# Kernel optimization log

Measured on AMD Instinct MI355X. Metric: run time of the kernel, lower is better.

The kernel has to match this reference:

```python
import jax, jax.numpy as jnp
import numpy as np

H, O, E, V = 128, 128, 512, 34
B, T, L = 64, 2048, 256


def _lstm(x, wih, whh, bih, bhh):
    # x: [T, B, Din] -> outputs [T, B, H]; PyTorch gate order i, f, g, o
    n = whh.shape[1]
    h0 = jnp.zeros((x.shape[1], n), x.dtype)
    b = bih + bhh
    def step(carry, xt):
        h, c = carry
        g = xt @ wih.T + h @ whh.T + b
        i, f, gg, o = jnp.split(g, 4, axis=-1)
        c = jax.nn.sigmoid(f) * c + jax.nn.sigmoid(i) * jnp.tanh(gg)
        h = jax.nn.sigmoid(o) * jnp.tanh(c)
        return (h, c), h
    _, ys = jax.lax.scan(step, (h0, h0), x)
    return ys


def _conv1d_s2(x, w, b):
    # x: [B, Cin, T], w: [Cout, Cin, 2], kernel=2 stride=2 valid
    y = jax.lax.conv_general_dilated(x, w, (2,), 'VALID', dimension_numbers=('NCH', 'OIH', 'NCH'))
    return y + b[None, :, None]


def setup_inputs():
    key = jax.random.key(0)
    ctr = [0]
    def mk(shape, s=0.05):
        ctr[0] += 1
        return jax.random.normal(jax.random.fold_in(key, ctr[0]), shape, dtype=jnp.float32) * s
    inp = {}
    inp['utter'] = mk((B, T, 40), 1.0)
    inp['targets'] = jax.random.randint(jax.random.fold_in(key, 999), (B, L), 0, V)
    inp['wih_f'] = mk((4 * H, 40)); inp['whh_f'] = mk((4 * H, H)); inp['bih_f'] = mk((4 * H,)); inp['bhh_f'] = mk((4 * H,))
    inp['wih_r'] = mk((4 * H, 40)); inp['whh_r'] = mk((4 * H, H)); inp['bih_r'] = mk((4 * H,)); inp['bhh_r'] = mk((4 * H,))
    inp['c1w'] = mk((H, 2 * H, 2)); inp['c1b'] = mk((H,))
    inp['wih1'] = mk((4 * H, H)); inp['whh1'] = mk((4 * H, H)); inp['bih1'] = mk((4 * H,)); inp['bhh1'] = mk((4 * H,))
    inp['c2w'] = mk((H, H, 2)); inp['c2b'] = mk((H,))
    inp['wih2'] = mk((4 * H, H)); inp['whh2'] = mk((4 * H, H)); inp['bih2'] = mk((4 * H,)); inp['bhh2'] = mk((4 * H,))
    inp['kw'] = mk((O, H)); inp['kb'] = mk((O,)); inp['vw'] = mk((O, H)); inp['vb'] = mk((O,))
    inp['wihd'] = mk((4 * O, O + E)); inp['whhd'] = mk((4 * O, O)); inp['bihd'] = mk((4 * O,)); inp['bhhd'] = mk((4 * O,))
    inp['w1'] = mk((V, O)); inp['b1'] = mk((V,)); inp['w2'] = mk((V, O)); inp['b2'] = mk((V,))
    inp['w3'] = mk((V, V)); inp['b3'] = mk((V,))
    inp['emb'] = mk((V, E), 1.0)
    inp['sh0'] = mk((B, O)); inp['sc0'] = mk((B, O))
    return inp


def _forward(utter, targets, wih_f, whh_f, bih_f, bhh_f, wih_r, whh_r, bih_r, bhh_r,
             c1w, c1b, wih1, whh1, bih1, bhh1, c2w, c2b, wih2, whh2, bih2, bhh2,
             kw, kb, vw, vb, wihd, whhd, bihd, bhhd, w1, b1, w2, b2, w3, b3,
             emb, sh0, sc0):
    # ---- Listener (encoder) ----
    x = jnp.transpose(utter, (1, 0, 2))            # [T, B, 40]
    fwd = _lstm(x, wih_f, whh_f, bih_f, bhh_f)
    bwd = _lstm(x[::-1], wih_r, whh_r, bih_r, bhh_r)[::-1]
    h = jnp.concatenate([fwd, bwd], axis=-1)       # [T, B, 2H]
    h = jnp.transpose(h, (1, 2, 0))                # [B, 2H, T]
    h = _conv1d_s2(h, c1w, c1b)                    # [B, H, T/2]
    h = jnp.transpose(h, (2, 0, 1))                # [T/2, B, H]
    h = _lstm(h, wih1, whh1, bih1, bhh1)
    h = jnp.transpose(h, (1, 2, 0))
    h = _conv1d_s2(h, c2w, c2b)                    # [B, H, T/4]
    h = jnp.transpose(h, (2, 0, 1))
    h = _lstm(h, wih2, whh2, bih2, bhh2)
    h = jnp.transpose(h, (1, 0, 2))                # [B, T/4, H]
    hk = h @ kw.T + kb                              # [B, T/4, O]
    hv = h @ vw.T + vb
    # ---- Speller (decoder) ----
    ys = jnp.transpose(emb[targets], (1, 0, 2))[:-1]   # [L-1, B, E]
    mask = jnp.ones((utter.shape[0], hk.shape[1]), utter.dtype)  # all full-length
    bd = bihd + bhhd
    def step(carry, y_in):
        c, sh, sc = carry
        g = jnp.concatenate([y_in, c], axis=1) @ wihd.T + sh @ whhd.T + bd
        i, f, gg, o = jnp.split(g, 4, axis=-1)
        sc_n = jax.nn.sigmoid(f) * sc + jax.nn.sigmoid(i) * jnp.tanh(gg)
        sh_n = jax.nn.sigmoid(o) * jnp.tanh(sc_n)
        # NOTE: original attends with the cell state sc (faithful to source)
        att = jax.nn.softmax(jnp.einsum('btd,bd->bt', hk, sc_n), axis=1) * mask
        att = att / jnp.sum(att, axis=1, keepdims=True)
        c_n = jnp.einsum('bt,btd->bd', att, hv)
        out = jax.nn.relu(sh_n @ w1.T + b1 + c_n @ w2.T + b2)
        out = jax.nn.softmax(out @ w3.T + b3, axis=1)
        return (c_n, sh_n, sc_n), out
    c0 = jnp.zeros_like(sh0)
    _, preds = jax.lax.scan(step, (c0, sh0, sc0), ys)
    return jnp.transpose(preds, (1, 0, 2))         # [B, L-1, V]


def reference(utter, targets, wih_f, whh_f, bih_f, bhh_f, wih_r, whh_r, bih_r, bhh_r,
              c1w, c1b, wih1, whh1, bih1, bhh1, c2w, c2b, wih2, whh2, bih2, bhh2,
              kw, kb, vw, vb, wihd, whhd, bihd, bhhd, w1, b1, w2, b2, w3, b3,
              emb, sh0, sc0):
    return _forward(utter, targets, wih_f, whh_f, bih_f, bhh_f, wih_r, whh_r, bih_r, bhh_r,
                    c1w, c1b, wih1, whh1, bih1, bhh1, c2w, c2b, wih2, whh2, bih2, bhh2,
                    kw, kb, vw, vb, wihd, whhd, bihd, bhhd, w1, b1, w2, b2, w3, b3,
                    emb, sh0, sc0)
```

## Files before the change

### kernel.cpp

```cpp
#include <hip/hip_runtime.h>

typedef _Float16 half_t;
typedef _Float16 __attribute__((ext_vector_type(2))) half2_t;

__device__ __forceinline__ float fdot2_(half2_t a, half2_t b, float c) {
#if __has_builtin(__builtin_amdgcn_fdot2)
    return __builtin_amdgcn_fdot2(a, b, c, false);
#else
    return c + (float)a[0] * (float)b[0] + (float)a[1] * (float)b[1];
#endif
}
__device__ __forceinline__ half2_t h2(float a, float b) {
    half2_t r; r[0] = (half_t)a; r[1] = (half_t)b; return r;
}
__device__ __forceinline__ half2_t bc2(unsigned int u) {
    return __builtin_bit_cast(half2_t, u);
}
__device__ __forceinline__ unsigned int pk2(float a, float b) {
    return __builtin_bit_cast(unsigned int, h2(a, b));
}
__device__ __forceinline__ float sigm(float x) { return 1.0f / (1.0f + __expf(-x)); }
__device__ __forceinline__ float tanh_(float x) { return 1.0f - 2.0f / (1.0f + __expf(2.0f * x)); }
__device__ __forceinline__ unsigned int packbf2(float a, float b) {
    unsigned int ua = __float_as_uint(a);
    ua = (ua + 0x7fffu + ((ua >> 16) & 1u)) >> 16;
    unsigned int ub = __float_as_uint(b);
    ub = (ub + 0x7fffu + ((ub >> 16) & 1u)) >> 16;
    return ua | (ub << 16);
}
__device__ __forceinline__ float blo(unsigned int u) { return __uint_as_float(u << 16); }
__device__ __forceinline__ float bhi(unsigned int u) { return __uint_as_float(u & 0xffff0000u); }

__global__ __launch_bounds__(512, 1) void lstm1_k(
    const float* __restrict__ utter,
    const float* __restrict__ wih_f, const float* __restrict__ whh_f,
    const float* __restrict__ bih_f, const float* __restrict__ bhh_f,
    const float* __restrict__ wih_r, const float* __restrict__ whh_r,
    const float* __restrict__ bih_r, const float* __restrict__ bhh_r,
    unsigned short* __restrict__ Hf, unsigned short* __restrict__ Hr)
{
    const int tid = threadIdx.x;
    const int b   = blockIdx.x & 63;
    const int dir = blockIdx.x >> 6;
    const float* wih = dir ? wih_r : wih_f;
    const float* whh = dir ? whh_r : whh_f;
    const float* bih = dir ? bih_r : bih_f;
    const float* bhh = dir ? bhh_r : bhh_f;
    unsigned short* Hout = dir ? Hr : Hf;

    __shared__ float acts[512];
    __shared__ __align__(16) half_t h_h[128];
    __shared__ __align__(16) half_t x2[3][48];

    const int j = tid;
    const int gt = tid >> 7;
    unsigned int wr2[64];
    {
        const float4* wp = reinterpret_cast<const float4*>(whh + j * 128);
#pragma unroll
        for (int m = 0; m < 32; ++m) {
            float4 v = wp[m];
            wr2[2 * m]     = pk2(v.x, v.y);
            wr2[2 * m + 1] = pk2(v.z, v.w);
        }
    }
    unsigned int wx2[20];
    {
        const float4* xp = reinterpret_cast<const float4*>(wih + j * 40);
#pragma unroll
        for (int q = 0; q < 10; ++q) {
            float4 v = xp[q];
            wx2[2 * q]     = pk2(v.x, v.y);
            wx2[2 * q + 1] = pk2(v.z, v.w);
        }
    }
    const float bias = bih[j] + bhh[j];
    float c = 0.0f;
    if (tid < 128) h_h[tid] = (half_t)0.0f;
    if (tid < 40) {
        int tt0 = dir ? 2047 : 0;
        x2[0][tid] = (half_t)utter[((size_t)b * 2048 + tt0) * 40 + tid];
    } else if (tid < 80) {
        int tt1 = dir ? 2046 : 1;
        x2[1][tid - 40] = (half_t)utter[((size_t)b * 2048 + tt1) * 40 + (tid - 40)];
    }
    __syncthreads();

    for (int t = 0; t < 2048; ++t) {
        const int cur = t % 3;
        const int nx2 = (t + 2) % 3;
        float xn = 0.0f;
        const int tq = tid - 128;
        if (tq >= 0 && tq < 40) {
            int tn = (t + 2 < 2048) ? (t + 2) : 2047;
            int ttn = dir ? (2047 - tn) : tn;
            xn = utter[((size_t)b * 2048 + ttn) * 40 + tq];
        }
        float g0 = bias, g1 = 0.f, g2 = 0.f, g3 = 0.f;
        {
            const uint4* x4p = reinterpret_cast<const uint4*>(&x2[cur][0]);
#pragma unroll
            for (int q = 0; q < 5; ++q) {
                uint4 u = x4p[q];
                g0 = fdot2_(bc2(wx2[4 * q]),     bc2(u.x), g0);
                g1 = fdot2_(bc2(wx2[4 * q + 1]), bc2(u.y), g1);
                g2 = fdot2_(bc2(wx2[4 * q + 2]), bc2(u.z), g2);
                g3 = fdot2_(bc2(wx2[4 * q + 3]), bc2(u.w), g3);
            }
            const uint4* h4p = reinterpret_cast<const uint4*>(h_h);
#pragma unroll
            for (int q = 0; q < 16; ++q) {
                uint4 u = h4p[q];
                g0 = fdot2_(bc2(wr2[4 * q]),     bc2(u.x), g0);
                g1 = fdot2_(bc2(wr2[4 * q + 1]), bc2(u.y), g1);
                g2 = fdot2_(bc2(wr2[4 * q + 2]), bc2(u.z), g2);
                g3 = fdot2_(bc2(wr2[4 * q + 3]), bc2(u.w), g3);
            }
        }
        float g = (g0 + g1) + (g2 + g3);
        acts[j] = (gt == 2) ? tanh_(g) : sigm(g);
        __syncthreads();
        if (tid < 128) {
            float i_ = acts[tid];
            float f_ = acts[128 + tid];
            float g_ = acts[256 + tid];
            float o_ = acts[384 + tid];
            c = f_ * c + i_ * g_;
            float hh = o_ * tanh_(c);
            half_t hx = (half_t)hh;
            h_h[tid] = hx;
            int tt = dir ? (2047 - t) : t;
            Hout[((size_t)tt * 64 + b) * 128 + tid] = __builtin_bit_cast(unsigned short, hx);
        } else if (tq < 40) {
            x2[nx2][tq] = (half_t)xn;
        }
        __syncthreads();
    }
}

__global__ __launch_bounds__(512, 1) void lstm_k(
    const unsigned short* __restrict__ Ph,
    const float* __restrict__ whh,
    void* __restrict__ Hout, int T, int outHalf)
{
    const int tid = threadIdx.x;
    const int b = blockIdx.x;
    const int j = tid;
    const int gt = tid >> 7;
    __shared__ float acts[512];
    __shared__ __align__(16) half_t h_h[128];
    unsigned int wr2[64];
    {
        const float4* wp = reinterpret_cast<const float4*>(whh + j * 128);
#pragma unroll
        for (int m = 0; m < 32; ++m) {
            float4 v = wp[m];
            wr2[2 * m]     = pk2(v.x, v.y);
            wr2[2 * m + 1] = pk2(v.z, v.w);
        }
    }
    float c = 0.0f;
    if (tid < 128) h_h[tid] = (half_t)0.0f;
    const size_t pbase = (size_t)b * T;
    float p_cur = (float)__builtin_bit_cast(half_t, Ph[(pbase + 0) * 512 + j]);
    float p_n1  = (float)__builtin_bit_cast(half_t, Ph[(pbase + 1) * 512 + j]);
    __syncthreads();
    for (int t = 0; t < T; ++t) {
        int tn = (t + 2 < T) ? (t + 2) : (T - 1);
        float p_n2 = (float)__builtin_bit_cast(half_t, Ph[(pbase + tn) * 512 + j]);
        float g0 = p_cur, g1 = 0.f, g2 = 0.f, g3 = 0.f;
        const uint4* h4p = reinterpret_cast<const uint4*>(h_h);
#pragma unroll
        for (int q = 0; q < 16; ++q) {
            uint4 u = h4p[q];
            g0 = fdot2_(bc2(wr2[4 * q]),     bc2(u.x), g0);
            g1 = fdot2_(bc2(wr2[4 * q + 1]), bc2(u.y), g1);
            g2 = fdot2_(bc2(wr2[4 * q + 2]), bc2(u.z), g2);
            g3 = fdot2_(bc2(wr2[4 * q + 3]), bc2(u.w), g3);
        }
        float g = (g0 + g1) + (g2 + g3);
        acts[j] = (gt == 2) ? tanh_(g) : sigm(g);
        __syncthreads();
        if (tid < 128) {
            float i_ = acts[tid];
            float f_ = acts[128 + tid];
            float g_ = acts[256 + tid];
            float o_ = acts[384 + tid];
            c = f_ * c + i_ * g_;
            float hh = o_ * tanh_(c);
            half_t hx = (half_t)hh;
            h_h[tid] = hx;
            size_t oi = ((size_t)t * 64 + b) * 128 + tid;
            if (outHalf) ((unsigned short*)Hout)[oi] = __builtin_bit_cast(unsigned short, hx);
            else         ((float*)Hout)[oi] = hh;
        }
        __syncthreads();
        p_cur = p_n1;
        p_n1 = p_n2;
    }
}

template <int CIN>
__global__ __launch_bounds__(128) void conv_k(
    const unsigned short* __restrict__ HA, const unsigned short* __restrict__ HB,
    const float* __restrict__ W, const float* __restrict__ bias,
    float* __restrict__ out, int Tout)
{
    __shared__ __align__(16) float xin[64 * CIN];
    const int b = blockIdx.x;
    const int t0 = blockIdx.y * 32;
    const int tid = threadIdx.x;
    for (int idx = tid; idx < 64 * CIN; idx += 128) {
        int tl = idx / CIN, ci = idx % CIN;
        int tau = t0 * 2 + tl;
        unsigned short u;
        if constexpr (CIN == 256) {
            u = (ci < 128) ? HA[(size_t)tau * 8192 + b * 128 + ci]
                           : HB[(size_t)tau * 8192 + b * 128 + (ci - 128)];
        } else {
            u = HA[(size_t)tau * 8192 + b * 128 + ci];
        }
        xin[idx] = (float)__builtin_bit_cast(half_t, u);
    }
    __syncthreads();
    const int co = tid;
    float acc[32];
#pragma unroll
    for (int u = 0; u < 32; ++u) acc[u] = 0.0f;
    const float4* Wrow4 = reinterpret_cast<const float4*>(W + (size_t)co * 2 * CIN);
    const float4* xin4 = reinterpret_cast<const float4*>(xin);
    for (int c4 = 0; c4 < CIN / 4; ++c4) {
        float4 wA = Wrow4[2 * c4];
        float4 wB = Wrow4[2 * c4 + 1];
#pragma unroll
        for (int u = 0; u < 32; ++u) {
            float4 x0 = xin4[(2 * u) * (CIN / 4) + c4];
            float4 x1 = xin4[(2 * u + 1) * (CIN / 4) + c4];
            acc[u] += wA.x * x0.x + wA.y * x1.x + wA.z * x0.y + wA.w * x1.y
                    + wB.x * x0.z + wB.y * x1.z + wB.z * x0.w + wB.w * x1.w;
        }
    }
    float bs = bias[co];
#pragma unroll
    for (int u = 0; u < 32; ++u)
        out[((size_t)b * Tout + t0 + u) * 128 + co] = acc[u] + bs;
}

__global__ __launch_bounds__(256) void gemm_k(
    const float* __restrict__ A, const float* __restrict__ W, int ldw,
    const float* __restrict__ bias1, const float* __restrict__ bias2,
    void* __restrict__ C, int M, int N, int K, int mode, int Tdim)
{
    __shared__ __align__(16) float As[16][68];
    __shared__ __align__(16) float Ws[16][68];
    const int tid = threadIdx.x;
    const int m0 = blockIdx.x * 64, n0 = blockIdx.y * 64;
    const int kk = tid & 15, mm = tid >> 4;
    const int tm = tid & 15, tn = tid >> 4;
    float acc[4][4];
#pragma unroll
    for (int i = 0; i < 4; ++i)
#pragma unroll
        for (int jj = 0; jj < 4; ++jj) acc[i][jj] = 0.0f;

    for (int k0 = 0; k0 < K; k0 += 16) {
#pragma unroll
        for (int r = 0; r < 4; ++r) {
            As[kk][mm + 16 * r] = A[(size_t)(m0 + mm + 16 * r) * K + k0 + kk];
            Ws[kk][mm + 16 * r] = W[(size_t)(n0 + mm + 16 * r) * ldw + k0 + kk];
        }
        __syncthreads();
#pragma unroll
        for (int q = 0; q < 16; ++q) {
            float4 a = reinterpret_cast<const float4*>(&As[q][0])[tm];
            float4 w = reinterpret_cast<const float4*>(&Ws[q][0])[tn];
            acc[0][0] += a.x * w.x; acc[0][1] += a.x * w.y; acc[0][2] += a.x * w.z; acc[0][3] += a.x * w.w;
            acc[1][0] += a.y * w.x; acc[1][1] += a.y * w.y; acc[1][2] += a.y * w.z; acc[1][3] += a.y * w.w;
            acc[2][0] += a.z * w.x; acc[2][1] += a.z * w.y; acc[2][2] += a.z * w.z; acc[2][3] += a.z * w.w;
            acc[3][0] += a.w * w.x; acc[3][1] += a.w * w.y; acc[3][2] += a.w * w.z; acc[3][3] += a.w * w.w;
        }
        __syncthreads();
    }
    float bv[4];
#pragma unroll
    for (int jj = 0; jj < 4; ++jj) {
        int n = n0 + tn * 4 + jj;
        float v = 0.0f;
        if (bias1) v += bias1[n];
        if (bias2) v += bias2[n];
        bv[jj] = v;
    }
#pragma unroll
    for (int i = 0; i < 4; ++i) {
        int m = m0 + tm * 4 + i;
#pragma unroll
        for (int jj = 0; jj < 4; ++jj) {
            int n = n0 + tn * 4 + jj;
            float v = acc[i][jj] + bv[jj];
            if (mode == 0) {
                ((float*)C)[(size_t)m * N + n] = v;
            } else if (mode == 1) {
                int bb = m & 63, tt = m >> 6;
                ((float*)C)[((size_t)bb * N + n) * Tdim + tt] = v;
            } else {
                ((unsigned short*)C)[(size_t)m * N + n] =
                    __builtin_bit_cast(unsigned short, (half_t)v);
            }
        }
    }
}

__global__ __launch_bounds__(512) void packemb_k(
    const int* __restrict__ targets, const float* __restrict__ emb,
    float* __restrict__ Ypack)
{
    int m = blockIdx.x;
    int l = m >> 6, b = m & 63;
    int tgt = targets[b * 256 + l];
    Ypack[(size_t)m * 512 + threadIdx.x] = emb[(size_t)tgt * 512 + threadIdx.x];
}

__global__ __launch_bounds__(256) void packq_k(
    const float* __restrict__ src, unsigned int* __restrict__ dst,
    int srcCols, int colOff, int nq, int rows)
{
    int g = blockIdx.x * 256 + threadIdx.x;
    if (g >= rows * nq * 4) return;
    int k = g & 3, t = g >> 2;
    int j = t % rows, q = t / rows;
    int p = q * 4 + k;
    const float* s = src + (size_t)j * srcCols + colOff + 2 * p;
    dst[g] = pk2(s[0], s[1]);
}

__global__ __launch_bounds__(1024) void packhv2_k(
    const float* __restrict__ hvT, unsigned int* __restrict__ hvq)
{
    int b = blockIdx.x;
    for (int it = 0; it < 32; ++it) {
        int idx = it * 1024 + threadIdx.x;
        int tq = idx >> 7, d = idx & 127;
        const float* s = hvT + ((size_t)b * 128 + d) * 512 + 2 * tq;
        hvq[(size_t)b * 32768 + idx] = packbf2(s[0], s[1]);
    }
}

__global__ __launch_bounds__(512, 1) void decoder_k(
    const float* __restrict__ Yp,
    const unsigned int* __restrict__ Wd,
    const float* __restrict__ hk,
    const unsigned int* __restrict__ hvq,
    const float* __restrict__ sh0, const float* __restrict__ sc0,
    float* __restrict__ SHs, float* __restrict__ Cs)
{
    __shared__ unsigned int hk_lds[512][66];
    __shared__ float acts[512];
    __shared__ float pfl[512];
    __shared__ __align__(16) half_t sh_h[128];
    __shared__ __align__(16) float sc_f[128];
    __shared__ __align__(16) half_t c_h[128];
    __shared__ __align__(16) float att[512];
    __shared__ float red[8];

    const int tid = threadIdx.x;
    const int b = blockIdx.x;
    const int gt = tid >> 7;

    uint4 wh[16];
    {
        const uint4* W4 = reinterpret_cast<const uint4*>(Wd);
#pragma unroll
        for (int q = 0; q < 16; ++q) wh[q] = W4[q * 512 + tid];
    }
    const uint4* Wc4 = reinterpret_cast<const uint4*>(Wd) + 8192;

    {
        const float4* hp = reinterpret_cast<const float4*>(hk + ((size_t)tid * 64 + b) * 128);
#pragma unroll
        for (int q = 0; q < 32; ++q) {
            float4 v = hp[q];
            hk_lds[tid][2 * q]     = packbf2(v.x, v.y);
            hk_lds[tid][2 * q + 1] = packbf2(v.z, v.w);
        }
    }
    float sc_r = 0.0f;
    if (tid < 128) {
        sh_h[tid] = (half_t)sh0[b * 128 + tid];
        sc_r = sc0[b * 128 + tid];
        sc_f[tid] = sc_r;
        c_h[tid] = (half_t)0.0f;
    }
    __syncthreads();

    const int wid = tid >> 6, lane = tid & 63;
    const int g4 = tid >> 7, d = tid & 127;
    const unsigned int* hvp = hvq + (size_t)b * 32768 + (size_t)(g4 * 64) * 128 + d;
    const float2* att2 = reinterpret_cast<const float2*>(att);
    float yp_cur = Yp[(size_t)b * 512 + tid];

    for (int l = 0; l < 255; ++l) {
        int lnxt = (l + 1 < 255) ? (l + 1) : l;
        float yp_nxt = Yp[((size_t)lnxt * 64 + b) * 512 + tid];
        {
            float g0 = yp_cur, g1 = 0.f, g2 = 0.f, g3 = 0.f;
            const uint4* s4 = reinterpret_cast<const uint4*>(sh_h);
#pragma unroll
            for (int q = 0; q < 16; ++q) {
                uint4 u = s4[q];
                g0 = fdot2_(bc2(wh[q].x), bc2(u.x), g0);
                g1 = fdot2_(bc2(wh[q].y), bc2(u.y), g1);
                g2 = fdot2_(bc2(wh[q].z), bc2(u.z), g2);
                g3 = fdot2_(bc2(wh[q].w), bc2(u.w), g3);
            }
            const uint4* c4 = reinterpret_cast<const uint4*>(c_h);
#pragma unroll
            for (int q = 0; q < 16; ++q) {
                uint4 w = Wc4[q * 512 + tid];
                uint4 u = c4[q];
                g0 = fdot2_(bc2(w.x), bc2(u.x), g0);
                g1 = fdot2_(bc2(w.y), bc2(u.y), g1);
                g2 = fdot2_(bc2(w.z), bc2(u.z), g2);
                g3 = fdot2_(bc2(w.w), bc2(u.w), g3);
            }
            float g = (g0 + g1) + (g2 + g3);
            acts[tid] = (gt == 2) ? tanh_(g) : sigm(g);
        }
        __syncthreads();
        if (tid < 128) {
            float i_ = acts[tid];
            float f_ = acts[128 + tid];
            float g_ = acts[256 + tid];
            float o_ = acts[384 + tid];
            sc_r = f_ * sc_r + i_ * g_;
            float hh = o_ * tanh_(sc_r);
            sh_h[tid] = (half_t)hh;
            sc_f[tid] = sc_r;
            SHs[((size_t)l * 64 + b) * 128 + tid] = hh;
        }
        __syncthreads();
        {
            float e0 = 0.f, e1 = 0.f, e2 = 0.f, e3 = 0.f;
            const uint2* hkr = reinterpret_cast<const uint2*>(&hk_lds[tid][0]);
            const float4* sc4 = reinterpret_cast<const float4*>(sc_f);
#pragma unroll
            for (int q = 0; q < 32; ++q) {
                uint2 u = hkr[q];
                float4 s = sc4[q];
                e0 += blo(u.x) * s.x; e1 += bhi(u.x) * s.y;
                e2 += blo(u.y) * s.z; e3 += bhi(u.y) * s.w;
            }
            float p = __expf((e0 + e1) + (e2 + e3));
            att[tid] = p;
            float ps = p;
#pragma unroll
            for (int off = 32; off; off >>= 1) ps += __shfl_xor(ps, off);
            if (lane == 0) red[wid] = ps;
        }
        __syncthreads();
        {
            float a0 = 0.f, a1 = 0.f;
#pragma unroll 8
            for (int i = 0; i < 64; i += 2) {
                unsigned int u0 = hvp[(size_t)i * 128];
                unsigned int u1 = hvp[(size_t)(i + 1) * 128];
                float2 w0 = att2[g4 * 64 + i];
                float2 w1 = att2[g4 * 64 + i + 1];
                a0 += blo(u0) * w0.x + bhi(u0) * w0.y;
                a1 += blo(u1) * w1.x + bhi(u1) * w1.y;
            }
            pfl[tid] = a0 + a1;
        }
        __syncthreads();
        if (tid < 128) {
            float S = ((red[0] + red[1]) + (red[2] + red[3]))
                    + ((red[4] + red[5]) + (red[6] + red[7]));
            float cv = (pfl[tid] + pfl[128 + tid] + pfl[256 + tid] + pfl[384 + tid]) / S;
            c_h[tid] = (half_t)cv;
            Cs[((size_t)l * 64 + b) * 128 + tid] = cv;
        }
        yp_cur = yp_nxt;
        __syncthreads();
    }
}

__global__ __launch_bounds__(256) void mlp_k(
    const float* __restrict__ SHs, const float* __restrict__ Cs,
    const float* __restrict__ w1, const float* __restrict__ b1,
    const float* __restrict__ w2, const float* __restrict__ b2,
    const float* __restrict__ w3, const float* __restrict__ b3,
    float* __restrict__ out)
{
    __shared__ float o_l[4][34];
    const int sub = threadIdx.x >> 6, lane = threadIdx.x & 63;
    const int m = blockIdx.x * 4 + sub;
    const int l = m >> 6, b = m & 63;
    if (lane < 34) {
        float o1 = b1[lane] + b2[lane];
        const float4* w1r = reinterpret_cast<const float4*>(w1 + lane * 128);
        const float4* w2r = reinterpret_cast<const float4*>(w2 + lane * 128);
        const float4* sh4 = reinterpret_cast<const float4*>(SHs + (size_t)m * 128);
        const float4* c4  = reinterpret_cast<const float4*>(Cs + (size_t)m * 128);
#pragma unroll 8
        for (int q = 0; q < 32; ++q) {
            float4 a = w1r[q], h = sh4[q], w = w2r[q], cc = c4[q];
            o1 += a.x * h.x + a.y * h.y + a.z * h.z + a.w * h.w
                + w.x * cc.x + w.y * cc.y + w.z * cc.z + w.w * cc.w;
        }
        o_l[sub][lane] = fmaxf(o1, 0.0f);
    }
    __syncthreads();
    if (lane < 34) {
        float zz = b3[lane];
        const float* w3r = w3 + lane * 34;
        for (int v = 0; v < 34; ++v) zz += w3r[v] * o_l[sub][v];
        __syncthreads();
        o_l[sub][lane] = zz;
        __syncthreads();
        float zm = o_l[sub][0];
        for (int v = 1; v < 34; ++v) zm = fmaxf(zm, o_l[sub][v]);
        float Ssum = 0.0f;
        for (int v = 0; v < 34; ++v) Ssum += __expf(o_l[sub][v] - zm);
        out[((size_t)b * 255 + l) * 34 + lane] = __expf(zz - zm) / Ssum;
    }
}

extern "C" void kernel_launch(void* const* d_in, const int* in_sizes, int n_in,
                              void* d_out, int out_size, void* d_ws, size_t ws_size,
                              hipStream_t stream) {
    (void)in_sizes; (void)n_in; (void)out_size; (void)ws_size;
    const float* utter = (const float*)d_in[0];
    const int*   targets = (const int*)d_in[1];
    const float* wih_f = (const float*)d_in[2];
    const float* whh_f = (const float*)d_in[3];
    const float* bih_f = (const float*)d_in[4];
    const float* bhh_f = (const float*)d_in[5];
    const float* wih_r = (const float*)d_in[6];
    const float* whh_r = (const float*)d_in[7];
    const float* bih_r = (const float*)d_in[8];
    const float* bhh_r = (const float*)d_in[9];
    const float* c1w = (const float*)d_in[10];
    const float* c1b = (const float*)d_in[11];
    const float* wih1 = (const float*)d_in[12];
    const float* whh1 = (const float*)d_in[13];
    const float* bih1 = (const float*)d_in[14];
    const float* bhh1 = (const float*)d_in[15];
    const float* c2w = (const float*)d_in[16];
    const float* c2b = (const float*)d_in[17];
    const float* wih2 = (const float*)d_in[18];
    const float* whh2 = (const float*)d_in[19];
    const float* bih2 = (const float*)d_in[20];
    const float* bhh2 = (const float*)d_in[21];
    const float* kw = (const float*)d_in[22];
    const float* kb = (const float*)d_in[23];
    const float* vw = (const float*)d_in[24];
    const float* vb = (const float*)d_in[25];
    const float* wihd = (const float*)d_in[26];
    const float* whhd = (const float*)d_in[27];
    const float* bihd = (const float*)d_in[28];
    const float* bhhd = (const float*)d_in[29];
    const float* w1 = (const float*)d_in[30];
    const float* b1 = (const float*)d_in[31];
    const float* w2 = (const float*)d_in[32];
    const float* b2 = (const float*)d_in[33];
    const float* w3 = (const float*)d_in[34];
    const float* b3 = (const float*)d_in[35];
    const float* emb = (const float*)d_in[36];
    const float* sh0 = (const float*)d_in[37];
    const float* sc0 = (const float*)d_in[38];

    char* ws = (char*)d_ws;
    const size_t MB = 1ull << 20;
    unsigned int* Wd = (unsigned int*)(ws + 0);

    unsigned short* Hf_h   = (unsigned short*)(ws + 1 * MB);
    unsigned short* Hr_h   = (unsigned short*)(ws + 33 * MB);
    float*          conv1o = (float*)(ws + 65 * MB);
    unsigned short* P2_h   = (unsigned short*)(ws + 1 * MB);
    unsigned short* H2_h   = (unsigned short*)(ws + 65 * MB);
    float*          conv2o = (float*)(ws + 81 * MB);
    unsigned short* P3_h   = (unsigned short*)(ws + 97 * MB);
    float*          H3     = (float*)(ws + 1 * MB);
    float*          hkb    = (float*)(ws + 17 * MB);
    float*          hvT    = (float*)(ws + 33 * MB);
    unsigned int*   hvq    = (unsigned int*)(ws + 49 * MB);
    float*          Ypack  = (float*)(ws + 57 * MB);
    float*          Yp     = (float*)(ws + 89 * MB);
    float*          SHsave = (float*)(ws + 121 * MB);
    float*          Csave  = (float*)(ws + 130 * MB);

    packq_k<<<128, 256, 0, stream>>>(whhd, Wd + 0,     128, 0,   16, 512);
    packq_k<<<128, 256, 0, stream>>>(wihd, Wd + 32768, 640, 512, 16, 512);

    lstm1_k<<<128, 512, 0, stream>>>(utter, wih_f, whh_f, bih_f, bhh_f,
                                     wih_r, whh_r, bih_r, bhh_r, Hf_h, Hr_h);
    conv_k<256><<<dim3(64, 32), 128, 0, stream>>>(Hf_h, Hr_h, c1w, c1b, conv1o, 1024);
    gemm_k<<<dim3(1024, 8), 256, 0, stream>>>(conv1o, wih1, 128, bih1, bhh1,
                                              P2_h, 65536, 512, 128, 2, 0);
    lstm_k<<<64, 512, 0, stream>>>(P2_h, whh1, H2_h, 1024, 1);
    conv_k<128><<<dim3(64, 16), 128, 0, stream>>>(H2_h, nullptr, c2w, c2b, conv2o, 512);
    gemm_k<<<dim3(512, 8), 256, 0, stream>>>(conv2o, wih2, 128, bih2, bhh2,
                                             P3_h, 32768, 512, 128, 2, 0);
    lstm_k<<<64, 512, 0, stream>>>(P3_h, whh2, H3, 512, 0);
    gemm_k<<<dim3(512, 2), 256, 0, stream>>>(H3, kw, 128, kb, nullptr,
                                             hkb, 32768, 128, 128, 0, 0);
    gemm_k<<<dim3(512, 2), 256, 0, stream>>>(H3, vw, 128, vb, nullptr,
                                             hvT, 32768, 128, 128, 1, 512);
    packhv2_k<<<64, 1024, 0, stream>>>(hvT, hvq);
    packemb_k<<<16320, 512, 0, stream>>>(targets, emb, Ypack);
    gemm_k<<<dim3(255, 8), 256, 0, stream>>>(Ypack, wihd, 640, bihd, bhhd,
                                             Yp, 16320, 512, 512, 0, 0);
    decoder_k<<<64, 512, 0, stream>>>(Yp, Wd, hkb, hvq, sh0, sc0, SHsave, Csave);
    mlp_k<<<4080, 256, 0, stream>>>(SHsave, Csave, w1, b1, w2, b2, w3, b3, (float*)d_out);
}
```

Before: 5.353 ms.

## Process two batch elements per block in the recurrent LSTM kernels

Each LSTM block now runs two batch sequences at once, so the per-thread weights held in registers are reused for both, and launches use half as many blocks. The goal is to amortise per-step barrier and weight costs across two sequences. In exchange, each thread does twice the dot-product and activation work per time step on the serial critical path. Because the GPU was already far from full with one batch per block, fewer blocks buy little and may lengthen each recurrent step.

```diff
diff --git a/kernel.cpp b/kernel.cpp
--- a/kernel.cpp
+++ b/kernel.cpp
@@ -40,17 +40,18 @@
     unsigned short* __restrict__ Hf, unsigned short* __restrict__ Hr)
 {
     const int tid = threadIdx.x;
-    const int b   = blockIdx.x & 63;
-    const int dir = blockIdx.x >> 6;
+    const int pair = blockIdx.x & 31;
+    const int dir  = blockIdx.x >> 5;
+    const int b0 = pair * 2;
     const float* wih = dir ? wih_r : wih_f;
     const float* whh = dir ? whh_r : whh_f;
     const float* bih = dir ? bih_r : bih_f;
     const float* bhh = dir ? bhh_r : bhh_f;
     unsigned short* Hout = dir ? Hr : Hf;
 
-    __shared__ float acts[512];
-    __shared__ __align__(16) half_t h_h[128];
-    __shared__ __align__(16) half_t x2[3][48];
+    __shared__ float acts[2][512];
+    __shared__ __align__(16) half_t h_h[2][128];
+    __shared__ __align__(16) half_t x3[3][2][48];
 
     const int j = tid;
     const int gt = tid >> 7;
@@ -76,13 +77,13 @@
     }
     const float bias = bih[j] + bhh[j];
     float c = 0.0f;
-    if (tid < 128) h_h[tid] = (half_t)0.0f;
-    if (tid < 40) {
-        int tt0 = dir ? 2047 : 0;
-        x2[0][tid] = (half_t)utter[((size_t)b * 2048 + tt0) * 40 + tid];
-    } else if (tid < 80) {
-        int tt1 = dir ? 2046 : 1;
-        x2[1][tid - 40] = (half_t)utter[((size_t)b * 2048 + tt1) * 40 + (tid - 40)];
+    if (tid < 256) h_h[tid >> 7][tid & 127] = (half_t)0.0f;
+    if (tid >= 256 && tid < 416) {
+        int u = tid - 256;
+        int sub = u / 80, rem = u % 80;
+        int row = rem / 40, col = rem % 40;
+        int tt = dir ? (2047 - row) : row;
+        x3[row][sub][col] = (half_t)utter[((size_t)(b0 + sub) * 2048 + tt) * 40 + col];
     }
     __syncthreads();
 
@@ -90,15 +91,16 @@
         const int cur = t % 3;
         const int nx2 = (t + 2) % 3;
         float xn = 0.0f;
-        const int tq = tid - 128;
-        if (tq >= 0 && tq < 40) {
+        const int tq = tid - 256;
+        const int psub = tq / 40, pcol = tq % 40;
+        if (tq >= 0 && tq < 80) {
             int tn = (t + 2 < 2048) ? (t + 2) : 2047;
             int ttn = dir ? (2047 - tn) : tn;
-            xn = utter[((size_t)b * 2048 + ttn) * 40 + tq];
-        }
-        float g0 = bias, g1 = 0.f, g2 = 0.f, g3 = 0.f;
+            xn = utter[((size_t)(b0 + psub) * 2048 + ttn) * 40 + pcol];
+        }
         {
-            const uint4* x4p = reinterpret_cast<const uint4*>(&x2[cur][0]);
+            float g0 = bias, g1 = 0.f, g2 = 0.f, g3 = 0.f;
+            const uint4* x4p = reinterpret_cast<const uint4*>(&x3[cur][0][0]);
 #pragma unroll
             for (int q = 0; q < 5; ++q) {
                 uint4 u = x4p[q];
@@ -107,7 +109,7 @@
                 g2 = fdot2_(bc2(wx2[4 * q + 2]), bc2(u.z), g2);
                 g3 = fdot2_(bc2(wx2[4 * q + 3]), bc2(u.w), g3);
             }
-            const uint4* h4p = reinterpret_cast<const uint4*>(h_h);
+            const uint4* h4p = reinterpret_cast<const uint4*>(&h_h[0][0]);
 #pragma unroll
             for (int q = 0; q < 16; ++q) {
                 uint4 u = h4p[q];
@@ -116,23 +118,47 @@
                 g2 = fdot2_(bc2(wr2[4 * q + 2]), bc2(u.z), g2);
                 g3 = fdot2_(bc2(wr2[4 * q + 3]), bc2(u.w), g3);
             }
-        }
-        float g = (g0 + g1) + (g2 + g3);
-        acts[j] = (gt == 2) ? tanh_(g) : sigm(g);
-        __syncthreads();
-        if (tid < 128) {
-            float i_ = acts[tid];
-            float f_ = acts[128 + tid];
-            float g_ = acts[256 + tid];
-            float o_ = acts[384 + tid];
+            float g = (g0 + g1) + (g2 + g3);
+            acts[0][j] = (gt == 2) ? tanh_(g) : sigm(g);
+        }
+        {
+            float g0 = bias, g1 = 0.f, g2 = 0.f, g3 = 0.f;
+            const uint4* x4p = reinterpret_cast<const uint4*>(&x3[cur][1][0]);
+#pragma unroll
+            for (int q = 0; q < 5; ++q) {
+                uint4 u = x4p[q];
+                g0 = fdot2_(bc2(wx2[4 * q]),     bc2(u.x), g0);
+                g1 = fdot2_(bc2(wx2[4 * q + 1]), bc2(u.y), g1);
+                g2 = fdot2_(bc2(wx2[4 * q + 2]), bc2(u.z), g2);
+                g3 = fdot2_(bc2(wx2[4 * q + 3]), bc2(u.w), g3);
+            }
+            const uint4* h4p = reinterpret_cast<const uint4*>(&h_h[1][0]);
+#pragma unroll
+            for (int q = 0; q < 16; ++q) {
+                uint4 u = h4p[q];
+                g0 = fdot2_(bc2(wr2[4 * q]),     bc2(u.x), g0);
+                g1 = fdot2_(bc2(wr2[4 * q + 1]), bc2(u.y), g1);
+                g2 = fdot2_(bc2(wr2[4 * q + 2]), bc2(u.z), g2);
+                g3 = fdot2_(bc2(wr2[4 * q + 3]), bc2(u.w), g3);
+            }
+            float g = (g0 + g1) + (g2 + g3);
+            acts[1][j] = (gt == 2) ? tanh_(g) : sigm(g);
+        }
+        __syncthreads();
+        if (tid < 256) {
+            int sub = tid >> 7, jj = tid & 127;
+            float i_ = acts[sub][jj];
+            float f_ = acts[sub][128 + jj];
+            float g_ = acts[sub][256 + jj];
+            float o_ = acts[sub][384 + jj];
             c = f_ * c + i_ * g_;
             float hh = o_ * tanh_(c);
             half_t hx = (half_t)hh;
-            h_h[tid] = hx;
+            h_h[sub][jj] = hx;
             int tt = dir ? (2047 - t) : t;
-            Hout[((size_t)tt * 64 + b) * 128 + tid] = __builtin_bit_cast(unsigned short, hx);
-        } else if (tq < 40) {
-            x2[nx2][tq] = (half_t)xn;
+            Hout[((size_t)tt * 64 + b0 + sub) * 128 + jj] = __builtin_bit_cast(unsigned short, hx);
+        } else if (tq < 80) {
+            x3[nx2][psub][pcol] = (half_t)xn;
         }
         __syncthreads();
     }
@@ -144,11 +170,11 @@
     void* __restrict__ Hout, int T, int outHalf)
 {
     const int tid = threadIdx.x;
-    const int b = blockIdx.x;
+    const int b0 = blockIdx.x * 2;
     const int j = tid;
     const int gt = tid >> 7;
-    __shared__ float acts[512];
-    __shared__ __align__(16) half_t h_h[128];
+    __shared__ float acts[2][512];
+    __shared__ __align__(16) half_t h_h[2][128];
     unsigned int wr2[64];
     {
         const float4* wp = reinterpret_cast<const float4*>(whh + j * 128);
@@ -160,43 +186,63 @@
         }
     }
     float c = 0.0f;
-    if (tid < 128) h_h[tid] = (half_t)0.0f;
-    const size_t pbase = (size_t)b * T;
-    float p_cur = (float)__builtin_bit_cast(half_t, Ph[(pbase + 0) * 512 + j]);
-    float p_n1  = (float)__builtin_bit_cast(half_t, Ph[(pbase + 1) * 512 + j]);
+    if (tid < 256) h_h[tid >> 7][tid & 127] = (half_t)0.0f;
+    const size_t pb0 = (size_t)b0 * T, pb1 = (size_t)(b0 + 1) * T;
+    float p0_cur = (float)__builtin_bit_cast(half_t, Ph[(pb0 + 0) * 512 + j]);
+    float p0_n1  = (float)__builtin_bit_cast(half_t, Ph[(pb0 + 1) * 512 + j]);
+    float p1_cur = (float)__builtin_bit_cast(half_t, Ph[(pb1 + 0) * 512 + j]);
+    float p1_n1  = (float)__builtin_bit_cast(half_t, Ph[(pb1 + 1) * 512 + j]);
     __syncthreads();
     for (int t = 0; t < T; ++t) {
         int tn = (t + 2 < T) ? (t + 2) : (T - 1);
-        float p_n2 = (float)__builtin_bit_cast(half_t, Ph[(pbase + tn) * 512 + j]);
-        float g0 = p_cur, g1 = 0.f, g2 = 0.f, g3 = 0.f;
-        const uint4* h4p = reinterpret_cast<const uint4*>(h_h);
-#pragma unroll
-        for (int q = 0; q < 16; ++q) {
-            uint4 u = h4p[q];
-            g0 = fdot2_(bc2(wr2[4 * q]),     bc2(u.x), g0);
-            g1 = fdot2_(bc2(wr2[4 * q + 1]), bc2(u.y), g1);
-            g2 = fdot2_(bc2(wr2[4 * q + 2]), bc2(u.z), g2);
-            g3 = fdot2_(bc2(wr2[4 * q + 3]), bc2(u.w), g3);
-        }
-        float g = (g0 + g1) + (g2 + g3);
-        acts[j] = (gt == 2) ? tanh_(g) : sigm(g);
-        __syncthreads();
-        if (tid < 128) {
-            float i_ = acts[tid];
-            float f_ = acts[128 + tid];
-            float g_ = acts[256 + tid];
-            float o_ = acts[384 + tid];
+        float p0_n2 = (float)__builtin_bit_cast(half_t, Ph[(pb0 + tn) * 512 + j]);
+        float p1_n2 = (float)__builtin_bit_cast(half_t, Ph[(pb1 + tn) * 512 + j]);
+        {
+            float g0 = p0_cur, g1 = 0.f, g2 = 0.f, g3 = 0.f;
+            const uint4* h4p = reinterpret_cast<const uint4*>(&h_h[0][0]);
+#pragma unroll
+            for (int q = 0; q < 16; ++q) {
+                uint4 u = h4p[q];
+                g0 = fdot2_(bc2(wr2[4 * q]),     bc2(u.x), g0);
+                g1 = fdot2_(bc2(wr2[4 * q + 1]), bc2(u.y), g1);
+                g2 = fdot2_(bc2(wr2[4 * q + 2]), bc2(u.z), g2);
+                g3 = fdot2_(bc2(wr2[4 * q + 3]), bc2(u.w), g3);
+            }
+            float g = (g0 + g1) + (g2 + g3);
+            acts[0][j] = (gt == 2) ? tanh_(g) : sigm(g);
+        }
+        {
+            float g0 = p1_cur, g1 = 0.f, g2 = 0.f, g3 = 0.f;
+            const uint4* h4p = reinterpret_cast<const uint4*>(&h_h[1][0]);
+#pragma unroll
+            for (int q = 0; q < 16; ++q) {
+                uint4 u = h4p[q];
+                g0 = fdot2_(bc2(wr2[4 * q]),     bc2(u.x), g0);
+                g1 = fdot2_(bc2(wr2[4 * q + 1]), bc2(u.y), g1);
+                g2 = fdot2_(bc2(wr2[4 * q + 2]), bc2(u.z), g2);
+                g3 = fdot2_(bc2(wr2[4 * q + 3]), bc2(u.w), g3);
+            }
+            float g = (g0 + g1) + (g2 + g3);
+            acts[1][j] = (gt == 2) ? tanh_(g) : sigm(g);
+        }
+        __syncthreads();
+        if (tid < 256) {
+            int sub = tid >> 7, jj = tid & 127;
+            float i_ = acts[sub][jj];
+            float f_ = acts[sub][128 + jj];
+            float g_ = acts[sub][256 + jj];
+            float o_ = acts[sub][384 + jj];
             c = f_ * c + i_ * g_;
             float hh = o_ * tanh_(c);
             half_t hx = (half_t)hh;
-            h_h[tid] = hx;
-            size_t oi = ((size_t)t * 64 + b) * 128 + tid;
+            h_h[sub][jj] = hx;
+            size_t oi = ((size_t)t * 64 + b0 + sub) * 128 + jj;
             if (outHalf) ((unsigned short*)Hout)[oi] = __builtin_bit_cast(unsigned short, hx);
             else         ((float*)Hout)[oi] = hh;
         }
         __syncthreads();
-        p_cur = p_n1;
-        p_n1 = p_n2;
+        p0_cur = p0_n1; p0_n1 = p0_n2;
+        p1_cur = p1_n1; p1_n1 = p1_n2;
     }
 }
 
@@ -591,16 +637,16 @@
     packq_k<<<128, 256, 0, stream>>>(whhd, Wd + 0,     128, 0,   16, 512);
     packq_k<<<128, 256, 0, stream>>>(wihd, Wd + 32768, 640, 512, 16, 512);
 
-    lstm1_k<<<128, 512, 0, stream>>>(utter, wih_f, whh_f, bih_f, bhh_f,
-                                     wih_r, whh_r, bih_r, bhh_r, Hf_h, Hr_h);
+    lstm1_k<<<64, 512, 0, stream>>>(utter, wih_f, whh_f, bih_f, bhh_f,
+                                    wih_r, whh_r, bih_r, bhh_r, Hf_h, Hr_h);
     conv_k<256><<<dim3(64, 32), 128, 0, stream>>>(Hf_h, Hr_h, c1w, c1b, conv1o, 1024);
     gemm_k<<<dim3(1024, 8), 256, 0, stream>>>(conv1o, wih1, 128, bih1, bhh1,
                                               P2_h, 65536, 512, 128, 2, 0);
-    lstm_k<<<64, 512, 0, stream>>>(P2_h, whh1, H2_h, 1024, 1);
+    lstm_k<<<32, 512, 0, stream>>>(P2_h, whh1, H2_h, 1024, 1);
     conv_k<128><<<dim3(64, 16), 128, 0, stream>>>(H2_h, nullptr, c2w, c2b, conv2o, 512);
     gemm_k<<<dim3(512, 8), 256, 0, stream>>>(conv2o, wih2, 128, bih2, bhh2,
                                              P3_h, 32768, 512, 128, 2, 0);
-    lstm_k<<<64, 512, 0, stream>>>(P3_h, whh2, H3, 512, 0);
+    lstm_k<<<32, 512, 0, stream>>>(P3_h, whh2, H3, 512, 0);
     gemm_k<<<dim3(512, 2), 256, 0, stream>>>(H3, kw, 128, kb, nullptr,
                                              hkb, 32768, 128, 128, 0, 0);
     gemm_k<<<dim3(512, 2), 256, 0, stream>>>(H3, vw, 128, vb, nullptr,
```

Result: slower. 7.304 ms (+36.5%).

## Batch LSTM hidden-state stores and input prefetch in 8-step chunks

Applied to the files above, without the earlier changes.

Both recurrent LSTM kernels now process time in chunks of 8 steps. Hidden outputs go into a shared-memory ring and are written to global memory once per chunk by all 512 threads as packed pairs, replacing per-step scalar 16-bit stores from 128 threads. Inputs (utter rows or precomputed gate projections) are prefetched a whole chunk ahead into registers or double-buffered shared memory instead of two steps ahead. This moves global traffic off the serial per-step critical path, at the cost of more shared memory, more live registers, and an extra barrier-free flush after each chunk. The flush assumes T is a multiple of 8.

```diff
diff --git a/kernel.cpp b/kernel.cpp
--- a/kernel.cpp
+++ b/kernel.cpp
@@ -50,7 +50,8 @@
 
     __shared__ float acts[512];
     __shared__ __align__(16) half_t h_h[128];
-    __shared__ __align__(16) half_t x2[3][48];
+    __shared__ __align__(16) half_t x2[2][8][48];
+    __shared__ __align__(16) float ring[8][128];
 
     const int j = tid;
     const int gt = tid >> 7;
@@ -77,36 +78,111 @@
     const float bias = bih[j] + bhh[j];
     float c = 0.0f;
     if (tid < 128) h_h[tid] = (half_t)0.0f;
-    if (tid < 40) {
-        int tt0 = dir ? 2047 : 0;
-        x2[0][tid] = (half_t)utter[((size_t)b * 2048 + tt0) * 40 + tid];
-    } else if (tid < 80) {
-        int tt1 = dir ? 2046 : 1;
-        x2[1][tid - 40] = (half_t)utter[((size_t)b * 2048 + tt1) * 40 + (tid - 40)];
+    const int xs = tid / 40, xc = tid % 40;
+    if (tid < 320) {
+        int tt0 = dir ? (2047 - xs) : xs;
+        x2[0][xs][xc] = (half_t)utter[((size_t)b * 2048 + tt0) * 40 + xc];
     }
     __syncthreads();
 
-    for (int t = 0; t < 2048; ++t) {
-        const int cur = t % 3;
-        const int nx2 = (t + 2) % 3;
-        float xn = 0.0f;
-        const int tq = tid - 128;
-        if (tq >= 0 && tq < 40) {
-            int tn = (t + 2 < 2048) ? (t + 2) : 2047;
+    for (int tc = 0; tc < 2048; tc += 8) {
+        const int ph = (tc >> 3) & 1;
+        float xreg = 0.0f;
+        if (tid < 320) {
+            int tn = tc + 8 + xs; if (tn > 2047) tn = 2047;
             int ttn = dir ? (2047 - tn) : tn;
-            xn = utter[((size_t)b * 2048 + ttn) * 40 + tq];
-        }
-        float g0 = bias, g1 = 0.f, g2 = 0.f, g3 = 0.f;
+            xreg = utter[((size_t)b * 2048 + ttn) * 40 + xc];
+        }
+#pragma unroll
+        for (int s = 0; s < 8; ++s) {
+            float g0 = bias, g1 = 0.f, g2 = 0.f, g3 = 0.f;
+            {
+                const uint4* x4p = reinterpret_cast<const uint4*>(&x2[ph][s][0]);
+#pragma unroll
+                for (int q = 0; q < 5; ++q) {
+                    uint4 u = x4p[q];
+                    g0 = fdot2_(bc2(wx2[4 * q]),     bc2(u.x), g0);
+                    g1 = fdot2_(bc2(wx2[4 * q + 1]), bc2(u.y), g1);
+                    g2 = fdot2_(bc2(wx2[4 * q + 2]), bc2(u.z), g2);
+                    g3 = fdot2_(bc2(wx2[4 * q + 3]), bc2(u.w), g3);
+                }
+                const uint4* h4p = reinterpret_cast<const uint4*>(h_h);
+#pragma unroll
+                for (int q = 0; q < 16; ++q) {
+                    uint4 u = h4p[q];
+                    g0 = fdot2_(bc2(wr2[4 * q]),     bc2(u.x), g0);
+                    g1 = fdot2_(bc2(wr2[4 * q + 1]), bc2(u.y), g1);
+                    g2 = fdot2_(bc2(wr2[4 * q + 2]), bc2(u.z), g2);
+                    g3 = fdot2_(bc2(wr2[4 * q + 3]), bc2(u.w), g3);
+                }
+            }
+            float g = (g0 + g1) + (g2 + g3);
+            acts[j] = (gt == 2) ? tanh_(g) : sigm(g);
+            __syncthreads();
+            if (s == 7 && tid < 320)
+                x2[ph ^ 1][xs][xc] = (half_t)xreg;
+            if (tid < 128) {
+                float i_ = acts[tid];
+                float f_ = acts[128 + tid];
+                float g_ = acts[256 + tid];
+                float o_ = acts[384 + tid];
+                c = f_ * c + i_ * g_;
+                float hh = o_ * tanh_(c);
+                h_h[tid] = (half_t)hh;
+                ring[s][tid] = hh;
+            }
+            __syncthreads();
+        }
         {
-            const uint4* x4p = reinterpret_cast<const uint4*>(&x2[cur][0]);
-#pragma unroll
-            for (int q = 0; q < 5; ++q) {
-                uint4 u = x4p[q];
-                g0 = fdot2_(bc2(wx2[4 * q]),     bc2(u.x), g0);
-                g1 = fdot2_(bc2(wx2[4 * q + 1]), bc2(u.y), g1);
-                g2 = fdot2_(bc2(wx2[4 * q + 2]), bc2(u.z), g2);
-                g3 = fdot2_(bc2(wx2[4 * q + 3]), bc2(u.w), g3);
-            }
+            int s2 = tid >> 6, pr = tid & 63;
+            int t = tc + s2;
+            int tt = dir ? (2047 - t) : t;
+            unsigned int v = pk2(ring[s2][2 * pr], ring[s2][2 * pr + 1]);
+            reinterpret_cast<unsigned int*>(Hout)[((size_t)tt * 64 + b) * 64 + pr] = v;
+        }
+    }
+}
+
+__global__ __launch_bounds__(512, 1) void lstm_k(
+    const unsigned short* __restrict__ Ph,
+    const float* __restrict__ whh,
+    void* __restrict__ Hout, int T, int outHalf)
+{
+    const int tid = threadIdx.x;
+    const int b = blockIdx.x;
+    const int j = tid;
+    const int gt = tid >> 7;
+    __shared__ float acts[512];
+    __shared__ __align__(16) half_t h_h[128];
+    __shared__ __align__(16) float ring[8][128];
+    unsigned int wr2[64];
+    {
+        const float4* wp = reinterpret_cast<const float4*>(whh + j * 128);
+#pragma unroll
+        for (int m = 0; m < 32; ++m) {
+            float4 v = wp[m];
+            wr2[2 * m]     = pk2(v.x, v.y);
+            wr2[2 * m + 1] = pk2(v.z, v.w);
+        }
+    }
+    float c = 0.0f;
+    if (tid < 128) h_h[tid] = (half_t)0.0f;
+    const size_t pbase = (size_t)b * T;
+    float pcur[8], pnext[8];
+#pragma unroll
+    for (int s = 0; s < 8; ++s)
+        pcur[s] = (float)__builtin_bit_cast(half_t, Ph[(pbase + s) * 512 + j]);
+    __syncthreads();
+
+    for (int tc = 0; tc < T; tc += 8) {
+#pragma unroll
+        for (int s = 0; s < 8; ++s) {
+            int tn = tc + 8 + s; if (tn > T - 1) tn = T - 1;
+            pnext[s] = (float)__builtin_bit_cast(half_t, Ph[(pbase + tn) * 512 + j]);
+        }
+#pragma unroll
+        for (int s = 0; s < 8; ++s) {
+            float g0 = pcur[s], g1 = 0.f, g2 = 0.f, g3 = 0.f;
             const uint4* h4p = reinterpret_cast<const uint4*>(h_h);
 #pragma unroll
             for (int q = 0; q < 16; ++q) {
@@ -116,87 +192,35 @@
                 g2 = fdot2_(bc2(wr2[4 * q + 2]), bc2(u.z), g2);
                 g3 = fdot2_(bc2(wr2[4 * q + 3]), bc2(u.w), g3);
             }
-        }
-        float g = (g0 + g1) + (g2 + g3);
-        acts[j] = (gt == 2) ? tanh_(g) : sigm(g);
-        __syncthreads();
-        if (tid < 128) {
-            float i_ = acts[tid];
-            float f_ = acts[128 + tid];
-            float g_ = acts[256 + tid];
-            float o_ = acts[384 + tid];
-            c = f_ * c + i_ * g_;
-            float hh = o_ * tanh_(c);
-            half_t hx = (half_t)hh;
-            h_h[tid] = hx;
-            int tt = dir ? (2047 - t) : t;
-            Hout[((size_t)tt * 64 + b) * 128 + tid] = __builtin_bit_cast(unsigned short, hx);
-        } else if (tq < 40) {
-            x2[nx2][tq] = (half_t)xn;
-        }
-        __syncthreads();
-    }
-}
-
-__global__ __launch_bounds__(512, 1) void lstm_k(
-    const unsigned short* __restrict__ Ph,
-    const float* __restrict__ whh,
-    void* __restrict__ Hout, int T, int outHalf)
-{
-    const int tid = threadIdx.x;
-    const int b = blockIdx.x;
-    const int j = tid;
-    const int gt = tid >> 7;
-    __shared__ float acts[512];
-    __shared__ __align__(16) half_t h_h[128];
-    unsigned int wr2[64];
-    {
-        const float4* wp = reinterpret_cast<const float4*>(whh + j * 128);
-#pragma unroll
-        for (int m = 0; m < 32; ++m) {
-            float4 v = wp[m];
-            wr2[2 * m]     = pk2(v.x, v.y);
-            wr2[2 * m + 1] = pk2(v.z, v.w);
-        }
-    }
-    float c = 0.0f;
-    if (tid < 128) h_h[tid] = (half_t)0.0f;
-    const size_t pbase = (size_t)b * T;
-    float p_cur = (float)__builtin_bit_cast(half_t, Ph[(pbase + 0) * 512 + j]);
-    float p_n1  = (float)__builtin_bit_cast(half_t, Ph[(pbase + 1) * 512 + j]);
-    __syncthreads();
-    for (int t = 0; t < T; ++t) {
-        int tn = (t + 2 < T) ? (t + 2) : (T - 1);
-        float p_n2 = (float)__builtin_bit_cast(half_t, Ph[(pbase + tn) * 512 + j]);
-        float g0 = p_cur, g1 = 0.f, g2 = 0.f, g3 = 0.f;
-        const uint4* h4p = reinterpret_cast<const uint4*>(h_h);
-#pragma unroll
-        for (int q = 0; q < 16; ++q) {
-            uint4 u = h4p[q];
-            g0 = fdot2_(bc2(wr2[4 * q]),     bc2(u.x), g0);
-            g1 = fdot2_(bc2(wr2[4 * q + 1]), bc2(u.y), g1);
-            g2 = fdot2_(bc2(wr2[4 * q + 2]), bc2(u.z), g2);
-            g3 = fdot2_(bc2(wr2[4 * q + 3]), bc2(u.w), g3);
-        }
-        float g = (g0 + g1) + (g2 + g3);
-        acts[j] = (gt == 2) ? tanh_(g) : sigm(g);
-        __syncthreads();
-        if (tid < 128) {
-            float i_ = acts[tid];
-            float f_ = acts[128 + tid];
-            float g_ = acts[256 + tid];
-            float o_ = acts[384 + tid];
-            c = f_ * c + i_ * g_;
-            float hh = o_ * tanh_(c);
-            half_t hx = (half_t)hh;
-            h_h[tid] = hx;
-            size_t oi = ((size_t)t * 64 + b) * 128 + tid;
-            if (outHalf) ((unsigned short*)Hout)[oi] = __builtin_bit_cast(unsigned short, hx);
-            else         ((float*)Hout)[oi] = hh;
-        }
-        __syncthreads();
-        p_cur = p_n1;
-        p_n1 = p_n2;
+            float g = (g0 + g1) + (g2 + g3);
+            acts[j] = (gt == 2) ? tanh_(g) : sigm(g);
+            __syncthreads();
+            if (tid < 128) {
+                float i_ = acts[tid];
+                float f_ = acts[128 + tid];
+                float g_ = acts[256 + tid];
+                float o_ = acts[384 + tid];
+                c = f_ * c + i_ * g_;
+                float hh = o_ * tanh_(c);
+                h_h[tid] = (half_t)hh;
+                ring[s][tid] = hh;
+            }
+            __syncthreads();
+        }
+        {
+            int s2 = tid >> 6, pr = tid & 63;
+            int t = tc + s2;
+            if (outHalf) {
+                unsigned int v = pk2(ring[s2][2 * pr], ring[s2][2 * pr + 1]);
+                reinterpret_cast<unsigned int*>(Hout)[((size_t)t * 64 + b) * 64 + pr] = v;
+            } else {
+                float2 v = make_float2(ring[s2][2 * pr], ring[s2][2 * pr + 1]);
+                *reinterpret_cast<float2*>(
+                    &reinterpret_cast<float*>(Hout)[((size_t)t * 64 + b) * 128 + 2 * pr]) = v;
+            }
+        }
+#pragma unroll
+        for (int s = 0; s < 8; ++s) pcur[s] = pnext[s];
     }
 }
 
```

Result: faster. 5.133 ms (-4.1%).
